# Performance work log

Hardware: AMD Instinct MI355X
Metric: run time of the kernel (lower is better)

Reference implementation:

```python
import jax, jax.numpy as jnp
import numpy as np

D_MODEL = 768; D_KV = 64; H = 12; D_FF = 3072; L = 2
TP = 4; SP = 16; MT = 16; MS = 4
MASK_RATE = 0.2; EPS = 1e-6
B = 256; T = 64; F = 64
ST = (T // TP) * (F // SP)  # 64 tokens


def ln(x, s, b):
    mu = jnp.mean(x, -1, keepdims=True)
    var = jnp.mean(jnp.square(x - mu), -1, keepdims=True)
    return (x - mu) * jax.lax.rsqrt(var + EPS) * s + b


def mha(x, Wq, bq, Wk, bk, Wv, bv, Wo, bo):
    Bz, S, D = x.shape
    q = (x @ Wq + bq).reshape(Bz, S, H, D_KV)
    k = (x @ Wk + bk).reshape(Bz, S, H, D_KV)
    v = (x @ Wv + bv).reshape(Bz, S, H, D_KV)
    scores = jnp.einsum('bqhd,bkhd->bhqk', q, k) * (D_KV ** -0.5)
    attn = jax.nn.softmax(scores, axis=-1)
    o = jnp.einsum('bhqk,bkhd->bqhd', attn, v).reshape(Bz, S, H * D_KV)
    return o @ Wo + bo


def setup_inputs():
    key = jax.random.key(0)
    ks = jax.random.split(key, 16)
    s = 0.02
    nrm = lambda k, shp: jax.random.normal(k, shp, jnp.float32) * s
    return {
        'inputs': jax.random.normal(ks[0], (B, T, F, 1), jnp.float32),
        'randomness': jax.random.uniform(ks[1], (B * ST, 3), jnp.float32),
        'perm': jax.random.permutation(ks[2], B * ST),
        'conv_w': nrm(ks[3], (TP, SP, 1, D_MODEL)), 'conv_b': jnp.zeros((D_MODEL,)),
        'temp_embd': nrm(ks[4], (MT, D_MODEL)), 'spec_embd': nrm(ks[5], (MS, D_MODEL)),
        'pos_ln_s': jnp.ones((D_MODEL,)), 'pos_ln_b': jnp.zeros((D_MODEL,)),
        'mask_tok': nrm(ks[6], (D_MODEL,)), 'agg_tok': nrm(ks[7], (D_MODEL,)),
        'Wq': nrm(ks[8], (L, D_MODEL, H * D_KV)), 'bq': jnp.zeros((L, H * D_KV)),
        'Wk': nrm(ks[9], (L, D_MODEL, H * D_KV)), 'bk': jnp.zeros((L, H * D_KV)),
        'Wv': nrm(ks[10], (L, D_MODEL, H * D_KV)), 'bv': jnp.zeros((L, H * D_KV)),
        'Wo': nrm(ks[11], (L, H * D_KV, D_MODEL)), 'bo': jnp.zeros((L, D_MODEL)),
        'ln1_s': jnp.ones((L, D_MODEL)), 'ln1_b': jnp.zeros((L, D_MODEL)),
        'W1': nrm(ks[12], (L, D_MODEL, D_FF)), 'b1': jnp.zeros((L, D_FF)),
        'W2': nrm(ks[13], (L, D_FF, D_MODEL)), 'b2': jnp.zeros((L, D_MODEL)),
        'ln2_s': jnp.ones((L, D_MODEL)), 'ln2_b': jnp.zeros((L, D_MODEL)),
    }


def reference(inputs, randomness, perm, conv_w, conv_b, temp_embd, spec_embd,
              pos_ln_s, pos_ln_b, mask_tok, agg_tok, Wq, bq, Wk, bk, Wv, bv,
              Wo, bo, ln1_s, ln1_b, W1, b1, W2, b2, ln2_s, ln2_b):
    # Conv2D patchify: [B, T, F, 1] -> [B, T/4, F/16, d_model]
    x = jax.lax.conv_general_dilated(
        inputs, conv_w, (TP, SP), 'VALID',
        dimension_numbers=('NHWC', 'HWIO', 'NHWC')) + conv_b
    Bz, Tt, Ss, D = x.shape
    e = x.reshape(Bz, Tt * Ss, D)  # token embeddings [B, 64, 768]
    # Vectorized BERT-style random masking (replaces the per-element sparse-scatter loop)
    sel = randomness[:, 0] <= MASK_RATE
    m = (sel & (randomness[:, 1] <= 0.8)).astype(e.dtype).reshape(Bz, Tt * Ss)
    rnd = (sel & (randomness[:, 1] > 0.8) & (randomness[:, 2] <= 0.5)).astype(e.dtype).reshape(Bz, Tt * Ss)
    shuffled = jax.lax.stop_gradient(e.reshape(-1, D))[perm].reshape(Bz, Tt * Ss, D)
    me = e * (1.0 - m - rnd)[..., None] + mask_tok * m[..., None] + shuffled * rnd[..., None]
    # Spectro-temporal position embeddings + LN
    pos = (temp_embd[:Tt, None, :] + spec_embd[None, :Ss, :]).reshape(Tt * Ss, D)
    h = ln(me + pos, pos_ln_s, pos_ln_b)
    # Prepend AGG token
    h = jnp.concatenate([jnp.broadcast_to(agg_tok, (Bz, 1, D)), h], axis=1)
    # Post-norm transformer encoder
    for l in range(L):
        a = mha(h, Wq[l], bq[l], Wk[l], bk[l], Wv[l], bv[l], Wo[l], bo[l])
        h = ln(h + a, ln1_s[l], ln1_b[l])
        f = jax.nn.gelu(h @ W1[l] + b1[l], approximate=False) @ W2[l] + b2[l]
        h = ln(h + f, ln2_s[l], ln2_b[l])
    return h  # last_hidden_states [B, 65, 768]; aggregated=h[:,0], predictions=h[:,1:]
```

## Files before the change

kernel.cpp:

```cpp
#include <hip/hip_runtime.h>
#include <hip/hip_bf16.h>
#include <math.h>

using bf16 = __hip_bfloat16;
typedef __bf16 bf16x8v __attribute__((ext_vector_type(8)));
typedef float f32x4 __attribute__((ext_vector_type(4)));
typedef unsigned short ushort4v __attribute__((ext_vector_type(4)));
typedef unsigned short ushort8v __attribute__((ext_vector_type(8)));

__device__ __forceinline__ float b2f(bf16 x) { return __bfloat162float(x); }
__device__ __forceinline__ bf16 f2b(float x) { return __float2bfloat16(x); }

__device__ __forceinline__ void gload_lds16(const void* g, void* l) {
  __builtin_amdgcn_global_load_lds(
      (__attribute__((address_space(1))) void*)(void*)g,
      (__attribute__((address_space(3))) void*)l, 16, 0, 0);
}

__device__ __forceinline__ float block_sum(float v, float* buf) {
  #pragma unroll
  for (int off = 32; off > 0; off >>= 1) v += __shfl_xor(v, off);
  __syncthreads();
  if ((threadIdx.x & 63) == 0) buf[threadIdx.x >> 6] = v;
  __syncthreads();
  return buf[0] + buf[1] + buf[2] + buf[3];
}

__global__ __launch_bounds__(256) void transpose_all_kernel(
    const float* __restrict__ Wq, const float* __restrict__ Wk,
    const float* __restrict__ Wv, const float* __restrict__ Wo,
    const float* __restrict__ W1, const float* __restrict__ W2,
    bf16* __restrict__ wqkvT, bf16* __restrict__ woT,
    bf16* __restrict__ w1T, bf16* __restrict__ w2T) {
  __shared__ float tile[32][33];
  const int tb = blockIdx.x;
  const float* src; bf16* dst; int K, N, t;
  if (tb < 4608) {
    const int job = tb / 576; t = tb % 576;
    const int l = job >> 2, c = job & 3;
    src = (c == 0 ? Wq : c == 1 ? Wk : c == 2 ? Wv : Wo) + (size_t)l * 768 * 768;
    dst = (c < 3) ? (wqkvT + (size_t)l * 2304 * 768 + (size_t)c * 768 * 768)
                  : (woT + (size_t)l * 768 * 768);
    K = 768; N = 768;
  } else if (tb < 9216) {
    const int r = tb - 4608; const int l = r / 2304; t = r % 2304;
    src = W1 + (size_t)l * 768 * 3072; dst = w1T + (size_t)l * 3072 * 768;
    K = 768; N = 3072;
  } else {
    const int r = tb - 9216; const int l = r / 2304; t = r % 2304;
    src = W2 + (size_t)l * 3072 * 768; dst = w2T + (size_t)l * 768 * 3072;
    K = 3072; N = 768;
  }
  const int nbx = N >> 5;
  const int bx = t % nbx, by = t / nbx;
  const int tx = threadIdx.x & 31, ty = threadIdx.x >> 5;
  #pragma unroll
  for (int i = 0; i < 4; ++i) {
    const int r = by * 32 + ty + i * 8;
    tile[ty + i * 8][tx] = src[(size_t)r * N + bx * 32 + tx];
  }
  __syncthreads();
  #pragma unroll
  for (int i = 0; i < 4; ++i) {
    const int r = bx * 32 + ty + i * 8;
    dst[(size_t)r * K + by * 32 + tx] = f2b(tile[tx][ty + i * 8]);
  }
}

__global__ __launch_bounds__(256) void biasqkv_kernel(
    const float* __restrict__ bq, const float* __restrict__ bk,
    const float* __restrict__ bv, float* __restrict__ out) {
  const int i = blockIdx.x * 256 + threadIdx.x;
  if (i >= 2 * 2304) return;
  const int l = i / 2304, n = i % 2304;
  float v = (n < 768) ? bq[l * 768 + n]
          : (n < 1536) ? bk[l * 768 + n - 768] : bv[l * 768 + n - 1536];
  out[i] = v;
}

__global__ __launch_bounds__(256) void patchify_kernel(
    const float* __restrict__ in, const float* __restrict__ w,
    const float* __restrict__ cb, bf16* __restrict__ e) {
  __shared__ float patch[8][64];
  const int tid = threadIdx.x;
  const int tok0 = blockIdx.x * 8;
  for (int idx = tid; idx < 512; idx += 256) {
    const int t = idx >> 6, p = idx & 63;
    const int tok = tok0 + t;
    const int b = tok >> 6, t2 = tok & 63, tt = t2 >> 2, ss = t2 & 3;
    const int kt = p >> 4, kf = p & 15;
    patch[t][p] = in[((size_t)b * 64 + tt * 4 + kt) * 64 + ss * 16 + kf];
  }
  __syncthreads();
  for (int i = 0; i < 3; ++i) {
    const int d = tid + i * 256;
    const float cbv = cb[d];
    float acc[8];
    #pragma unroll
    for (int t = 0; t < 8; ++t) acc[t] = cbv;
    for (int p = 0; p < 64; ++p) {
      const float wv = w[p * 768 + d];
      #pragma unroll
      for (int t = 0; t < 8; ++t) acc[t] += patch[t][p] * wv;
    }
    #pragma unroll
    for (int t = 0; t < 8; ++t) e[(size_t)(tok0 + t) * 768 + d] = f2b(acc[t]);
  }
}

__global__ __launch_bounds__(256) void embed_kernel(
    const bf16* __restrict__ e, const float* __restrict__ randomness,
    const int* __restrict__ perm, const float* __restrict__ temp_embd,
    const float* __restrict__ spec_embd, const float* __restrict__ pls,
    const float* __restrict__ plb, const float* __restrict__ mask_tok,
    const float* __restrict__ agg_tok, bf16* __restrict__ h) {
  __shared__ float rbuf[4];
  const int row = blockIdx.x;
  const int b = row / 65, s = row % 65;
  const int tid = threadIdx.x;
  const size_t ob = (size_t)row * 768;
  if (s == 0) {
    #pragma unroll
    for (int i = 0; i < 3; ++i) { const int d = tid + i * 256; h[ob + d] = f2b(agg_tok[d]); }
    return;
  }
  const int tok = s - 1;
  const int gt = b * 64 + tok;
  const float r0 = randomness[gt * 3 + 0];
  const float r1 = randomness[gt * 3 + 1];
  const float r2 = randomness[gt * 3 + 2];
  const bool selb = (r0 <= 0.2f);
  const bool mflag = selb && (r1 <= 0.8f);
  const bool rflag = selb && (r1 > 0.8f) && (r2 <= 0.5f);
  const int src = rflag ? perm[gt] : gt;
  const int tt = tok >> 2, ss2 = tok & 3;
  float v[3]; float sum = 0.f;
  #pragma unroll
  for (int i = 0; i < 3; ++i) {
    const int d = tid + i * 256;
    const float ev = mflag ? mask_tok[d] : b2f(e[(size_t)src * 768 + d]);
    v[i] = ev + temp_embd[tt * 768 + d] + spec_embd[ss2 * 768 + d];
    sum += v[i];
  }
  const float mu = block_sum(sum, rbuf) * (1.f / 768.f);
  float q = 0.f;
  #pragma unroll
  for (int i = 0; i < 3; ++i) { const float t = v[i] - mu; q += t * t; }
  const float rstd = rsqrtf(block_sum(q, rbuf) * (1.f / 768.f) + 1e-6f);
  #pragma unroll
  for (int i = 0; i < 3; ++i) {
    const int d = tid + i * 256;
    h[ob + d] = f2b((v[i] - mu) * rstd * pls[d] + plb[d]);
  }
}

template <int F32OUT>
__global__ __launch_bounds__(256) void resln_kernel(
    const bf16* __restrict__ x, const bf16* __restrict__ y,
    const float* __restrict__ sc, const float* __restrict__ bi,
    void* __restrict__ outp) {
  __shared__ float rbuf[4];
  const int tid = threadIdx.x;
  const size_t base = (size_t)blockIdx.x * 768;
  float v[3]; float s = 0.f;
  #pragma unroll
  for (int i = 0; i < 3; ++i) {
    const int d = tid + i * 256;
    v[i] = b2f(x[base + d]) + b2f(y[base + d]);
    s += v[i];
  }
  const float mu = block_sum(s, rbuf) * (1.f / 768.f);
  float q = 0.f;
  #pragma unroll
  for (int i = 0; i < 3; ++i) { const float t = v[i] - mu; q += t * t; }
  const float rstd = rsqrtf(block_sum(q, rbuf) * (1.f / 768.f) + 1e-6f);
  #pragma unroll
  for (int i = 0; i < 3; ++i) {
    const int d = tid + i * 256;
    const float o = (v[i] - mu) * rstd * sc[d] + bi[d];
    if (F32OUT) ((float*)outp)[base + d] = o;
    else        ((bf16*)outp)[base + d] = f2b(o);
  }
}

template <int ACT>
__global__ __launch_bounds__(256, 4) void gemm128_kernel(
    const unsigned short* __restrict__ A, const unsigned short* __restrict__ BT,
    const float* __restrict__ bias, bf16* __restrict__ C, int N, int K, int nbn) {
  constexpr int SLOT = 16384;
  __shared__ __align__(16) char smem[2 * SLOT];

  const int nwg = gridDim.x;
  const int orig = blockIdx.x;
  const int q8 = nwg >> 3, r8 = nwg & 7;
  const int xcd = orig & 7, lin = orig >> 3;
  const int bid = (xcd < r8 ? xcd * (q8 + 1) : r8 * (q8 + 1) + (xcd - r8) * q8) + lin;
  const int bm = bid / nbn, bn = bid % nbn;

  const int tid = threadIdx.x;
  const int w = tid >> 6, lane = tid & 63;
  const int wm = (w >> 1) * 64, wn = (w & 1) * 64;
  const int frow = lane & 15;
  const int cg = lane >> 4;
  const int rdCB = ((cg ^ ((frow >> 1) & 3)) << 4);

  const size_t Kb = (size_t)K * 2;
  const int srow = lane >> 2;
  const int srcCB = (((lane & 3) ^ ((lane >> 3) & 3)) << 4);
  const char* gA = (const char*)A + ((size_t)bm * 128 + w * 16 + srow) * Kb + srcCB;
  const char* gB = (const char*)BT + ((size_t)bn * 128 + w * 16 + srow) * Kb + srcCB;

  f32x4 acc[4][4];
  #pragma unroll
  for (int i = 0; i < 4; ++i)
    #pragma unroll
    for (int j = 0; j < 4; ++j) acc[i][j] = f32x4{0.f, 0.f, 0.f, 0.f};

  auto stage = [&](int t, int slotIdx) {
    char* sa = smem + slotIdx * SLOT;
    char* sb = sa + 8192;
    const size_t kb = (size_t)t * 64;
    gload_lds16(gA + kb, sa + w * 1024);
    gload_lds16(gA + (size_t)64 * Kb + kb, sa + 4096 + w * 1024);
    gload_lds16(gB + kb, sb + w * 1024);
    gload_lds16(gB + (size_t)64 * Kb + kb, sb + 4096 + w * 1024);
  };

  auto compute = [&](int slotIdx) {
    const char* sa = smem + slotIdx * SLOT;
    const char* sb = sa + 8192;
    bf16x8v aa[4], bb[4];
    #pragma unroll
    for (int m = 0; m < 4; ++m)
      aa[m] = *(const bf16x8v*)(sa + (wm + m * 16 + frow) * 64 + rdCB);
    #pragma unroll
    for (int n = 0; n < 4; ++n)
      bb[n] = *(const bf16x8v*)(sb + (wn + n * 16 + frow) * 64 + rdCB);
    __builtin_amdgcn_s_setprio(1);
    #pragma unroll
    for (int m = 0; m < 4; ++m)
      #pragma unroll
      for (int n = 0; n < 4; ++n)
        acc[m][n] = __builtin_amdgcn_mfma_f32_16x16x32_bf16(aa[m], bb[n], acc[m][n], 0, 0, 0);
    __builtin_amdgcn_s_setprio(0);
  };

  const int T = K >> 5;
  stage(0, 0);
  __syncthreads();
  int cur = 0;
  for (int t = 0; t < T; ++t) {
    if (t + 1 < T) stage(t + 1, cur ^ 1);
    compute(cur);
    __syncthreads();
    cur ^= 1;
  }

  bf16* cbuf = (bf16*)smem;
  float bias4[4];
  #pragma unroll
  for (int n = 0; n < 4; ++n) bias4[n] = bias[bn * 128 + wn + n * 16 + frow];
  const int rgrp = (lane >> 4) << 2;
  #pragma unroll
  for (int half = 0; half < 2; ++half) {
    if ((w >> 1) == half) {
      #pragma unroll
      for (int mf = 0; mf < 4; ++mf)
        #pragma unroll
        for (int n = 0; n < 4; ++n) {
          const int col = wn + n * 16 + frow;
          #pragma unroll
          for (int r = 0; r < 4; ++r) {
            float v = acc[mf][n][r] + bias4[n];
            if (ACT == 1) v = 0.5f * v * (1.0f + erff(v * 0.70710678f));
            cbuf[(mf * 16 + rgrp + r) * 136 + col] = f2b(v);
          }
        }
    }
    __syncthreads();
    #pragma unroll
    for (int jj = 0; jj < 4; ++jj) {
      const int idx = tid + jj * 256;
      const int rowl = idx >> 4, c = idx & 15;
      const ushort8v val = *(const ushort8v*)(cbuf + rowl * 136 + c * 8);
      *(ushort8v*)(C + ((size_t)(bm * 128 + half * 64 + rowl)) * N + (size_t)bn * 128 + c * 8) = val;
    }
    __syncthreads();
  }
}

__global__ __launch_bounds__(320) void attn_mfma_kernel(
    const bf16* __restrict__ qkv, bf16* __restrict__ ctx) {
  __shared__ __align__(16) bf16 sK[80][72];
  __shared__ __align__(16) bf16 sVt[64][104];
  __shared__ __align__(16) bf16 sP[5][16][104];
  const int b = blockIdx.x / 12, h = blockIdx.x % 12;
  const int tid = threadIdx.x;
  const int wave = tid >> 6, lane = tid & 63;
  const size_t base = ((size_t)b * 65) * 2304 + (size_t)h * 64;
  const bf16 bzero = f2b(0.f);

  for (int idx = tid; idx < 65 * 16; idx += 320) {
    const int row = idx >> 4, d4 = (idx & 15) * 4;
    const ushort4v kv = *(const ushort4v*)(qkv + base + (size_t)row * 2304 + 768 + d4);
    const ushort4v vv = *(const ushort4v*)(qkv + base + (size_t)row * 2304 + 1536 + d4);
    *(ushort4v*)&sK[row][d4] = kv;
    #pragma unroll
    for (int j = 0; j < 4; ++j) ((unsigned short*)&sVt[d4 + j][row])[0] = vv[j];
  }
  for (int idx = tid; idx < 15 * 16; idx += 320) {
    const int row = 65 + (idx >> 4), d4 = (idx & 15) * 4;
    *(ushort4v*)&sK[row][d4] = ushort4v{0, 0, 0, 0};
  }
  for (int idx = tid; idx < 64 * 31; idx += 320) {
    const int d = idx / 31, c = 65 + (idx % 31);
    sVt[d][c] = bzero;
  }
  __syncthreads();

  const int frow = lane & 15;
  const int koff = (lane >> 4) * 8;
  const int row0 = wave * 16;
  const int qrow = (row0 + frow > 64) ? 64 : (row0 + frow);
  const bf16* qptr = qkv + base + (size_t)qrow * 2304;
  const bf16x8v aq0 = *(const bf16x8v*)(qptr + koff);
  const bf16x8v aq1 = *(const bf16x8v*)(qptr + 32 + koff);

  const f32x4 z4 = {0.f, 0.f, 0.f, 0.f};
  f32x4 sacc[5];
  #pragma unroll
  for (int n = 0; n < 5; ++n) sacc[n] = z4;
  #pragma unroll
  for (int n = 0; n < 5; ++n) {
    const bf16x8v b0 = *(const bf16x8v*)&sK[n * 16 + frow][koff];
    const bf16x8v b1 = *(const bf16x8v*)&sK[n * 16 + frow][32 + koff];
    sacc[n] = __builtin_amdgcn_mfma_f32_16x16x32_bf16(aq0, b0, sacc[n], 0, 0, 0);
    sacc[n] = __builtin_amdgcn_mfma_f32_16x16x32_bf16(aq1, b1, sacc[n], 0, 0, 0);
  }

  #pragma unroll
  for (int r = 0; r < 4; ++r) {
    const int prow = ((lane >> 4) << 2) + r;
    float v[5];
    float mx = -1e30f;
    #pragma unroll
    for (int n = 0; n < 5; ++n) {
      const int col = n * 16 + frow;
      v[n] = (col < 65) ? sacc[n][r] * 0.125f : -1e30f;
      mx = fmaxf(mx, v[n]);
    }
    #pragma unroll
    for (int off = 1; off < 16; off <<= 1) mx = fmaxf(mx, __shfl_xor(mx, off));
    float sum = 0.f;
    #pragma unroll
    for (int n = 0; n < 5; ++n) { v[n] = __expf(v[n] - mx); sum += v[n]; }
    #pragma unroll
    for (int off = 1; off < 16; off <<= 1) sum += __shfl_xor(sum, off);
    const float inv = 1.f / sum;
    #pragma unroll
    for (int n = 0; n < 5; ++n)
      sP[wave][prow][n * 16 + frow] = f2b(v[n] * inv);
    sP[wave][prow][80 + frow] = bzero;
  }

  f32x4 oacc[4];
  #pragma unroll
  for (int n = 0; n < 4; ++n) oacc[n] = z4;
  #pragma unroll
  for (int kk = 0; kk < 3; ++kk) {
    const bf16x8v ap = *(const bf16x8v*)&sP[wave][frow][kk * 32 + koff];
    #pragma unroll
    for (int n = 0; n < 4; ++n) {
      const bf16x8v bv = *(const bf16x8v*)&sVt[n * 16 + frow][kk * 32 + koff];
      oacc[n] = __builtin_amdgcn_mfma_f32_16x16x32_bf16(ap, bv, oacc[n], 0, 0, 0);
    }
  }

  #pragma unroll
  for (int r = 0; r < 4; ++r) {
    const int row = row0 + ((lane >> 4) << 2) + r;
    if (row < 65) {
      bf16* op = ctx + ((size_t)b * 65 + row) * 768 + (size_t)h * 64 + frow;
      #pragma unroll
      for (int n = 0; n < 4; ++n) op[n * 16] = f2b(oacc[n][r]);
    }
  }
}

extern "C" void kernel_launch(void* const* d_in, const int* in_sizes, int n_in,
                              void* d_out, int out_size, void* d_ws, size_t ws_size,
                              hipStream_t stream) {
  (void)in_sizes; (void)n_in; (void)out_size; (void)ws_size;
  const float* inputs     = (const float*)d_in[0];
  const float* randomness = (const float*)d_in[1];
  const int*   perm       = (const int*)d_in[2];
  const float* conv_w     = (const float*)d_in[3];
  const float* conv_b     = (const float*)d_in[4];
  const float* temp_embd  = (const float*)d_in[5];
  const float* spec_embd  = (const float*)d_in[6];
  const float* pos_ln_s   = (const float*)d_in[7];
  const float* pos_ln_b   = (const float*)d_in[8];
  const float* mask_tok   = (const float*)d_in[9];
  const float* agg_tok    = (const float*)d_in[10];
  const float* Wq = (const float*)d_in[11]; const float* bq = (const float*)d_in[12];
  const float* Wk = (const float*)d_in[13]; const float* bk = (const float*)d_in[14];
  const float* Wv = (const float*)d_in[15]; const float* bv = (const float*)d_in[16];
  const float* Wo = (const float*)d_in[17]; const float* bo = (const float*)d_in[18];
  const float* ln1_s = (const float*)d_in[19]; const float* ln1_b = (const float*)d_in[20];
  const float* W1 = (const float*)d_in[21]; const float* b1 = (const float*)d_in[22];
  const float* W2 = (const float*)d_in[23]; const float* b2 = (const float*)d_in[24];
  const float* ln2_s = (const float*)d_in[25]; const float* ln2_b = (const float*)d_in[26];

  char* wsb = (char*)d_ws;
  size_t off = 0;
  auto carve = [&](size_t bytes) { char* p = wsb + off; off = (off + bytes + 255) & ~(size_t)255; return p; };
  bf16* wqkvT = (bf16*)carve((size_t)2 * 2304 * 768 * 2);
  bf16* woT   = (bf16*)carve((size_t)2 * 768 * 768 * 2);
  bf16* w1T   = (bf16*)carve((size_t)2 * 3072 * 768 * 2);
  bf16* w2T   = (bf16*)carve((size_t)2 * 768 * 3072 * 2);
  float* bqkv = (float*)carve((size_t)2 * 2304 * 4);
  bf16* ebuf  = (bf16*)carve((size_t)16640 * 768 * 2);
  bf16* hbuf  = (bf16*)carve((size_t)16640 * 768 * 2);
  bf16* qkvb  = (bf16*)carve((size_t)16640 * 2304 * 2);
  bf16* ctxb  = (bf16*)carve((size_t)16640 * 768 * 2);
  bf16* tmpb  = ebuf;
  bf16* midb  = qkvb;

  const dim3 blk(256);
  transpose_all_kernel<<<13824, blk, 0, stream>>>(Wq, Wk, Wv, Wo, W1, W2,
                                                  wqkvT, woT, w1T, w2T);
  biasqkv_kernel<<<18, blk, 0, stream>>>(bq, bk, bv, bqkv);
  patchify_kernel<<<2048, blk, 0, stream>>>(inputs, conv_w, conv_b, ebuf);
  embed_kernel<<<16640, blk, 0, stream>>>(ebuf, randomness, perm, temp_embd, spec_embd,
                                          pos_ln_s, pos_ln_b, mask_tok, agg_tok, hbuf);
  for (int l = 0; l < 2; ++l) {
    gemm128_kernel<0><<<130 * 18, blk, 0, stream>>>(
        (const unsigned short*)hbuf, (const unsigned short*)(wqkvT + (size_t)l * 2304 * 768),
        bqkv + l * 2304, qkvb, 2304, 768, 18);
    attn_mfma_kernel<<<256 * 12, dim3(320), 0, stream>>>(qkvb, ctxb);
    gemm128_kernel<0><<<130 * 6, blk, 0, stream>>>(
        (const unsigned short*)ctxb, (const unsigned short*)(woT + (size_t)l * 768 * 768),
        bo + l * 768, tmpb, 768, 768, 6);
    resln_kernel<0><<<16640, blk, 0, stream>>>(hbuf, tmpb, ln1_s + l * 768, ln1_b + l * 768, hbuf);
    gemm128_kernel<1><<<130 * 24, blk, 0, stream>>>(
        (const unsigned short*)hbuf, (const unsigned short*)(w1T + (size_t)l * 3072 * 768),
        b1 + l * 3072, midb, 3072, 768, 24);
    gemm128_kernel<0><<<130 * 6, blk, 0, stream>>>(
        (const unsigned short*)midb, (const unsigned short*)(w2T + (size_t)l * 768 * 3072),
        b2 + l * 768, tmpb, 768, 3072, 6);
    if (l == 1)
      resln_kernel<1><<<16640, blk, 0, stream>>>(hbuf, tmpb, ln2_s + l * 768, ln2_b + l * 768, d_out);
    else
      resln_kernel<0><<<16640, blk, 0, stream>>>(hbuf, tmpb, ln2_s + l * 768, ln2_b + l * 768, hbuf);
  }
}
```

Measured before the change: 949.9 us.

## Add 256x256-tile 8-wave pipelined GEMM for QKV and FFN1 projections

Introduces a 512-thread GEMM kernel with 256x256 output tiles, a 128KB double-buffered LDS staging scheme, and interleaved async global-to-LDS loads spread across MFMA phases with explicit waitcnt and barriers. It replaces the 128x128 GEMM for the wide QKV and FFN-up projections. The aim is higher arithmetic intensity and better overlap of loads with MFMA work. The cost is lower occupancy and fewer workgroups (585 and 780), which may leave the tail underused on a device with many CUs. The epilogue goes through LDS in two halves.

```diff
diff --git a/kernel.cpp b/kernel.cpp
--- a/kernel.cpp
+++ b/kernel.cpp
@@ -184,6 +184,141 @@
 }
 
 template <int ACT>
+__global__ __launch_bounds__(512, 2) void gemm8p2_kernel(
+    const unsigned short* __restrict__ A, const unsigned short* __restrict__ BT,
+    const float* __restrict__ bias, bf16* __restrict__ C, int N, int K, int nbn) {
+  __shared__ __align__(16) char smem[131072];
+
+  const int nwg = gridDim.x;
+  const int orig = blockIdx.x;
+  const int q8 = nwg >> 3, r8 = nwg & 7;
+  const int xcd = orig & 7, lin = orig >> 3;
+  const int bid = (xcd < r8 ? xcd * (q8 + 1) : r8 * (q8 + 1) + (xcd - r8) * q8) + lin;
+  const int bm = bid / nbn, bn = bid % nbn;
+
+  const int tid = threadIdx.x;
+  const int w = tid >> 6, lane = tid & 63;
+  const int wrow = w >> 2, wcol = w & 3;
+  const int frow = lane & 15;
+  const int cg = lane >> 4;
+  const int rdCB = ((cg ^ ((frow >> 1) & 3)) << 4);
+
+  const size_t Kb = (size_t)K * 2;
+  const int g_lr = lane >> 2;
+  const int srcCB = (((lane & 3) ^ ((lane >> 3) & 3)) << 4);
+  const char* gA = (const char*)A + ((size_t)bm * 256 + w * 16 + g_lr) * Kb + srcCB;
+  const char* gB = (const char*)BT + ((size_t)bn * 256 + w * 16 + g_lr) * Kb + srcCB;
+
+  f32x4 acc[8][4];
+  #pragma unroll
+  for (int i = 0; i < 8; ++i)
+    #pragma unroll
+    for (int j = 0; j < 4; ++j) acc[i][j] = f32x4{0.f, 0.f, 0.f, 0.f};
+
+  auto stageU = [&](int tc, int isB, int h) {
+    char* dst = smem + (tc & 1) * 65536 + isB * 32768 + h * 16384 + w * 1024;
+    const char* g = (isB ? gB : gA) + (size_t)tc * 128 + (size_t)h * 64;
+    gload_lds16(g, dst);
+    gload_lds16(g + (size_t)128 * Kb, dst + 8192);
+  };
+
+  stageU(0, 0, 0); stageU(0, 0, 1); stageU(0, 1, 0); stageU(0, 1, 1);
+  stageU(1, 1, 0); stageU(1, 1, 1);
+
+  const int nIter = K >> 7;
+  bf16x8v bb[4][2];
+
+  for (int i = 0; i < nIter; ++i) {
+    const int t0 = 2 * i;
+    const bool pf = (i + 1 < nIter);
+    #pragma unroll
+    for (int p = 0; p < 8; ++p) {
+      const int sl = p >> 2;
+      const int q = p & 3;
+      const char* slotp = smem + sl * 65536;
+      bf16x8v aa[2][2];
+      if (q == 0) {
+        if (p == 4 && !pf) { asm volatile("s_waitcnt vmcnt(0)" ::: "memory"); }
+        else               { asm volatile("s_waitcnt vmcnt(4)" ::: "memory"); }
+        __builtin_amdgcn_s_barrier();
+        #pragma unroll
+        for (int n = 0; n < 4; ++n) {
+          const int row = wcol * 64 + n * 16 + frow;
+          bb[n][0] = *(const bf16x8v*)(slotp + 32768 + row * 64 + rdCB);
+          bb[n][1] = *(const bf16x8v*)(slotp + 49152 + row * 64 + rdCB);
+        }
+        #pragma unroll
+        for (int j = 0; j < 2; ++j) {
+          const int row = wrow * 128 + j * 16 + frow;
+          aa[j][0] = *(const bf16x8v*)(slotp + row * 64 + rdCB);
+          aa[j][1] = *(const bf16x8v*)(slotp + 16384 + row * 64 + rdCB);
+        }
+        if (p == 0) stageU(t0 + 1, 0, 0);
+        else if (pf) stageU(t0 + 2, 0, 0);
+      } else {
+        #pragma unroll
+        for (int j = 0; j < 2; ++j) {
+          const int row = wrow * 128 + q * 32 + j * 16 + frow;
+          aa[j][0] = *(const bf16x8v*)(slotp + row * 64 + rdCB);
+          aa[j][1] = *(const bf16x8v*)(slotp + 16384 + row * 64 + rdCB);
+        }
+        if (p == 1) stageU(t0 + 1, 0, 1);
+        else if (p == 2) { if (pf) stageU(t0 + 2, 1, 0); }
+        else if (p == 3) { if (pf) stageU(t0 + 2, 1, 1); }
+        else if (p == 5) { if (pf) stageU(t0 + 2, 0, 1); }
+        else if (p == 6) { if (pf) stageU(t0 + 3, 1, 0); }
+        else             { if (pf) stageU(t0 + 3, 1, 1); }
+        __builtin_amdgcn_s_barrier();
+      }
+      asm volatile("s_waitcnt lgkmcnt(0)" ::: "memory");
+      __builtin_amdgcn_sched_barrier(0);
+      __builtin_amdgcn_s_setprio(1);
+      #pragma unroll
+      for (int j = 0; j < 2; ++j)
+        #pragma unroll
+        for (int n = 0; n < 4; ++n) {
+          acc[q * 2 + j][n] = __builtin_amdgcn_mfma_f32_16x16x32_bf16(aa[j][0], bb[n][0], acc[q * 2 + j][n], 0, 0, 0);
+          acc[q * 2 + j][n] = __builtin_amdgcn_mfma_f32_16x16x32_bf16(aa[j][1], bb[n][1], acc[q * 2 + j][n], 0, 0, 0);
+        }
+      __builtin_amdgcn_s_setprio(0);
+    }
+  }
+  __syncthreads();
+
+  bf16* cbuf = (bf16*)smem;
+  float bias4[4];
+  #pragma unroll
+  for (int n = 0; n < 4; ++n) bias4[n] = bias[bn * 256 + wcol * 64 + n * 16 + frow];
+  const int rgrp = (lane >> 4) << 2;
+  #pragma unroll
+  for (int half = 0; half < 2; ++half) {
+    if (wrow == half) {
+      #pragma unroll
+      for (int mf = 0; mf < 8; ++mf)
+        #pragma unroll
+        for (int n = 0; n < 4; ++n) {
+          const int col = wcol * 64 + n * 16 + frow;
+          #pragma unroll
+          for (int r = 0; r < 4; ++r) {
+            float v = acc[mf][n][r] + bias4[n];
+            if (ACT == 1) v = 0.5f * v * (1.0f + erff(v * 0.70710678f));
+            cbuf[(mf * 16 + rgrp + r) * 264 + col] = f2b(v);
+          }
+        }
+    }
+    __syncthreads();
+    #pragma unroll
+    for (int jj = 0; jj < 8; ++jj) {
+      const int idx = tid + jj * 512;
+      const int rowl = idx >> 5, c = idx & 31;
+      const ushort8v val = *(const ushort8v*)(cbuf + rowl * 264 + c * 8);
+      *(ushort8v*)(C + ((size_t)(bm * 256 + half * 128 + rowl)) * N + (size_t)bn * 256 + c * 8) = val;
+    }
+    __syncthreads();
+  }
+}
+
+template <int ACT>
 __global__ __launch_bounds__(256, 4) void gemm128_kernel(
     const unsigned short* __restrict__ A, const unsigned short* __restrict__ BT,
     const float* __restrict__ bias, bf16* __restrict__ C, int N, int K, int nbn) {
@@ -434,17 +569,17 @@
   embed_kernel<<<16640, blk, 0, stream>>>(ebuf, randomness, perm, temp_embd, spec_embd,
                                           pos_ln_s, pos_ln_b, mask_tok, agg_tok, hbuf);
   for (int l = 0; l < 2; ++l) {
-    gemm128_kernel<0><<<130 * 18, blk, 0, stream>>>(
+    gemm8p2_kernel<0><<<65 * 9, dim3(512), 0, stream>>>(
         (const unsigned short*)hbuf, (const unsigned short*)(wqkvT + (size_t)l * 2304 * 768),
-        bqkv + l * 2304, qkvb, 2304, 768, 18);
+        bqkv + l * 2304, qkvb, 2304, 768, 9);
     attn_mfma_kernel<<<256 * 12, dim3(320), 0, stream>>>(qkvb, ctxb);
     gemm128_kernel<0><<<130 * 6, blk, 0, stream>>>(
         (const unsigned short*)ctxb, (const unsigned short*)(woT + (size_t)l * 768 * 768),
         bo + l * 768, tmpb, 768, 768, 6);
     resln_kernel<0><<<16640, blk, 0, stream>>>(hbuf, tmpb, ln1_s + l * 768, ln1_b + l * 768, hbuf);
-    gemm128_kernel<1><<<130 * 24, blk, 0, stream>>>(
+    gemm8p2_kernel<1><<<65 * 12, dim3(512), 0, stream>>>(
         (const unsigned short*)hbuf, (const unsigned short*)(w1T + (size_t)l * 3072 * 768),
-        b1 + l * 3072, midb, 3072, 768, 24);
+        b1 + l * 3072, midb, 3072, 768, 12);
     gemm128_kernel<0><<<130 * 6, blk, 0, stream>>>(
         (const unsigned short*)midb, (const unsigned short*)(w2T + (size_t)l * 768 * 3072),
         b2 + l * 768, tmpb, 768, 3072, 6);
```

Result: slower. 1.096 ms (+15.4%).

## Add 256x128-tile GEMM using 32x32x16 MFMA for QKV and FFN1 projections

Applied to the files above, without the earlier changes.

Adds a new GEMM kernel with a 256x128 output tile per workgroup. Each wave computes a 128x64 sub-tile using 32x32x16 bf16 MFMA instructions, with K-step 32 double-buffered through LDS via direct global-to-LDS loads. It replaces the 128x128 GEMM for the QKV and W1 (GELU) projections, aiming for more operand reuse per LDS byte and fewer, larger MFMA ops. The cost is more accumulator registers and lower occupancy (launch bounds 2), plus a two-pass epilogue that stages output through shared memory.

```diff
diff --git a/kernel.cpp b/kernel.cpp
--- a/kernel.cpp
+++ b/kernel.cpp
@@ -5,6 +5,7 @@
 using bf16 = __hip_bfloat16;
 typedef __bf16 bf16x8v __attribute__((ext_vector_type(8)));
 typedef float f32x4 __attribute__((ext_vector_type(4)));
+typedef float f32x16 __attribute__((ext_vector_type(16)));
 typedef unsigned short ushort4v __attribute__((ext_vector_type(4)));
 typedef unsigned short ushort8v __attribute__((ext_vector_type(8)));
 
@@ -184,6 +185,128 @@
 }
 
 template <int ACT>
+__global__ __launch_bounds__(256, 2) void gemm32_kernel(
+    const unsigned short* __restrict__ A, const unsigned short* __restrict__ BT,
+    const float* __restrict__ bias, bf16* __restrict__ C, int N, int K, int nbn) {
+  constexpr int ABYTES = 256 * 64;
+  constexpr int BBYTES = 128 * 64;
+  constexpr int SLOT = ABYTES + BBYTES;
+  __shared__ __align__(16) char smem[2 * SLOT];
+
+  const int nwg = gridDim.x;
+  const int orig = blockIdx.x;
+  const int q8 = nwg >> 3, r8 = nwg & 7;
+  const int xcd = orig & 7, lin = orig >> 3;
+  const int bid = (xcd < r8 ? xcd * (q8 + 1) : r8 * (q8 + 1) + (xcd - r8) * q8) + lin;
+  const int bm = bid / nbn, bn = bid % nbn;
+
+  const int tid = threadIdx.x;
+  const int w = tid >> 6, lane = tid & 63;
+  const int wrow = w >> 1, wcol = w & 1;
+  const int lrow = lane & 31;
+  const int khl = lane >> 5;
+
+  const size_t Kb = (size_t)K * 2;
+  const int g_lr = lane >> 2;
+  const int srcCB = (((lane & 3) ^ ((lane >> 3) & 3)) << 4);
+  const char* gA = (const char*)A + ((size_t)bm * 256 + w * 16 + g_lr) * Kb + srcCB;
+  const char* gB = (const char*)BT + ((size_t)bn * 128 + w * 16 + g_lr) * Kb + srcCB;
+
+  f32x16 acc[4][2];
+  #pragma unroll
+  for (int i = 0; i < 4; ++i)
+    #pragma unroll
+    for (int j = 0; j < 2; ++j)
+      #pragma unroll
+      for (int r = 0; r < 16; ++r) acc[i][j][r] = 0.f;
+
+  auto stage = [&](int t, int slotIdx) {
+    char* sa = smem + slotIdx * SLOT;
+    char* sb = sa + ABYTES;
+    const size_t kb = (size_t)t * 64;
+    #pragma unroll
+    for (int j = 0; j < 4; ++j)
+      gload_lds16(gA + (size_t)j * 64 * Kb + kb, sa + j * 4096 + w * 1024);
+    #pragma unroll
+    for (int j = 0; j < 2; ++j)
+      gload_lds16(gB + (size_t)j * 64 * Kb + kb, sb + j * 4096 + w * 1024);
+  };
+
+  auto compute = [&](int slotIdx) {
+    const char* sa = smem + slotIdx * SLOT;
+    const char* sb = sa + ABYTES;
+    __builtin_amdgcn_s_setprio(1);
+    #pragma unroll
+    for (int h = 0; h < 2; ++h) {
+      bf16x8v aa[4], bb[2];
+      #pragma unroll
+      for (int mi = 0; mi < 4; ++mi) {
+        const int row = wrow * 128 + mi * 32 + lrow;
+        const int chunk = (h * 2 + khl) ^ ((row >> 1) & 3);
+        aa[mi] = *(const bf16x8v*)(sa + row * 64 + chunk * 16);
+      }
+      #pragma unroll
+      for (int ni = 0; ni < 2; ++ni) {
+        const int row = wcol * 64 + ni * 32 + lrow;
+        const int chunk = (h * 2 + khl) ^ ((row >> 1) & 3);
+        bb[ni] = *(const bf16x8v*)(sb + row * 64 + chunk * 16);
+      }
+      #pragma unroll
+      for (int mi = 0; mi < 4; ++mi)
+        #pragma unroll
+        for (int ni = 0; ni < 2; ++ni)
+          acc[mi][ni] = __builtin_amdgcn_mfma_f32_32x32x16_bf16(
+              aa[mi], bb[ni], acc[mi][ni], 0, 0, 0);
+    }
+    __builtin_amdgcn_s_setprio(0);
+  };
+
+  const int T = K >> 5;
+  stage(0, 0);
+  __syncthreads();
+  int cur = 0;
+  for (int t = 0; t < T; ++t) {
+    if (t + 1 < T) stage(t + 1, cur ^ 1);
+    compute(cur);
+    __syncthreads();
+    cur ^= 1;
+  }
+
+  bf16* cbuf = (bf16*)smem;
+  float bias2[2];
+  #pragma unroll
+  for (int ni = 0; ni < 2; ++ni)
+    bias2[ni] = bias[bn * 128 + wcol * 64 + ni * 32 + lrow];
+  #pragma unroll
+  for (int half = 0; half < 2; ++half) {
+    if (wrow == half) {
+      #pragma unroll
+      for (int mi = 0; mi < 4; ++mi)
+        #pragma unroll
+        for (int ni = 0; ni < 2; ++ni) {
+          const int col = wcol * 64 + ni * 32 + lrow;
+          #pragma unroll
+          for (int r = 0; r < 16; ++r) {
+            const int rowf = (r & 3) + 8 * (r >> 2) + 4 * khl;
+            float v = acc[mi][ni][r] + bias2[ni];
+            if (ACT == 1) v = 0.5f * v * (1.0f + erff(v * 0.70710678f));
+            cbuf[(mi * 32 + rowf) * 136 + col] = f2b(v);
+          }
+        }
+    }
+    __syncthreads();
+    #pragma unroll
+    for (int jj = 0; jj < 8; ++jj) {
+      const int idx = tid + jj * 256;
+      const int rowl = idx >> 4, c = idx & 15;
+      const ushort8v val = *(const ushort8v*)(cbuf + rowl * 136 + c * 8);
+      *(ushort8v*)(C + ((size_t)(bm * 256 + half * 128 + rowl)) * N + (size_t)bn * 128 + c * 8) = val;
+    }
+    __syncthreads();
+  }
+}
+
+template <int ACT>
 __global__ __launch_bounds__(256, 4) void gemm128_kernel(
     const unsigned short* __restrict__ A, const unsigned short* __restrict__ BT,
     const float* __restrict__ bias, bf16* __restrict__ C, int N, int K, int nbn) {
@@ -434,7 +557,7 @@
   embed_kernel<<<16640, blk, 0, stream>>>(ebuf, randomness, perm, temp_embd, spec_embd,
                                           pos_ln_s, pos_ln_b, mask_tok, agg_tok, hbuf);
   for (int l = 0; l < 2; ++l) {
-    gemm128_kernel<0><<<130 * 18, blk, 0, stream>>>(
+    gemm32_kernel<0><<<65 * 18, blk, 0, stream>>>(
         (const unsigned short*)hbuf, (const unsigned short*)(wqkvT + (size_t)l * 2304 * 768),
         bqkv + l * 2304, qkvb, 2304, 768, 18);
     attn_mfma_kernel<<<256 * 12, dim3(320), 0, stream>>>(qkvb, ctxb);
@@ -442,7 +565,7 @@
         (const unsigned short*)ctxb, (const unsigned short*)(woT + (size_t)l * 768 * 768),
         bo + l * 768, tmpb, 768, 768, 6);
     resln_kernel<0><<<16640, blk, 0, stream>>>(hbuf, tmpb, ln1_s + l * 768, ln1_b + l * 768, hbuf);
-    gemm128_kernel<1><<<130 * 24, blk, 0, stream>>>(
+    gemm32_kernel<1><<<65 * 24, blk, 0, stream>>>(
         (const unsigned short*)hbuf, (const unsigned short*)(w1T + (size_t)l * 3072 * 768),
         b1 + l * 3072, midb, 3072, 768, 24);
     gemm128_kernel<0><<<130 * 6, blk, 0, stream>>>(
```

Result: slower. 1.139 ms (+19.9%).

## Switch GEMM to single-buffered BK=64 tiles with 8-way XOR swizzle

Applied to the files above, without the earlier changes.

The GEMM kernel's K-tile grows from 32 to 64, and the double-buffered pipeline is replaced by one 32KB buffer holding A and B tiles. Each iteration now loads, syncs, computes two MFMA k-steps, then syncs again, and the LDS layout uses a 128-byte row with an 8-way XOR swizzle. This halves the number of loop iterations and barriers per unit of K. In exchange, global loads no longer overlap compute within a block, so the kernel relies on the four blocks per CU to hide that latency.

```diff
diff --git a/kernel.cpp b/kernel.cpp
--- a/kernel.cpp
+++ b/kernel.cpp
@@ -184,11 +184,10 @@
 }
 
 template <int ACT>
-__global__ __launch_bounds__(256, 4) void gemm128_kernel(
+__global__ __launch_bounds__(256, 4) void gemmbk64_kernel(
     const unsigned short* __restrict__ A, const unsigned short* __restrict__ BT,
     const float* __restrict__ bias, bf16* __restrict__ C, int N, int K, int nbn) {
-  constexpr int SLOT = 16384;
-  __shared__ __align__(16) char smem[2 * SLOT];
+  __shared__ __align__(16) char smem[32768];
 
   const int nwg = gridDim.x;
   const int orig = blockIdx.x;
@@ -202,13 +201,12 @@
   const int wm = (w >> 1) * 64, wn = (w & 1) * 64;
   const int frow = lane & 15;
   const int cg = lane >> 4;
-  const int rdCB = ((cg ^ ((frow >> 1) & 3)) << 4);
 
   const size_t Kb = (size_t)K * 2;
-  const int srow = lane >> 2;
-  const int srcCB = (((lane & 3) ^ ((lane >> 3) & 3)) << 4);
-  const char* gA = (const char*)A + ((size_t)bm * 128 + w * 16 + srow) * Kb + srcCB;
-  const char* gB = (const char*)BT + ((size_t)bn * 128 + w * 16 + srow) * Kb + srcCB;
+  const int laneRow8 = lane >> 3;
+  const int srcCB = (((lane & 7) ^ laneRow8) << 4);
+  const char* gA = (const char*)A + ((size_t)bm * 128 + w * 32 + laneRow8) * Kb + srcCB;
+  const char* gB = (const char*)BT + ((size_t)bn * 128 + w * 32 + laneRow8) * Kb + srcCB;
 
   f32x4 acc[4][4];
   #pragma unroll
@@ -216,44 +214,48 @@
     #pragma unroll
     for (int j = 0; j < 4; ++j) acc[i][j] = f32x4{0.f, 0.f, 0.f, 0.f};
 
-  auto stage = [&](int t, int slotIdx) {
-    char* sa = smem + slotIdx * SLOT;
-    char* sb = sa + 8192;
-    const size_t kb = (size_t)t * 64;
-    gload_lds16(gA + kb, sa + w * 1024);
-    gload_lds16(gA + (size_t)64 * Kb + kb, sa + 4096 + w * 1024);
-    gload_lds16(gB + kb, sb + w * 1024);
-    gload_lds16(gB + (size_t)64 * Kb + kb, sb + 4096 + w * 1024);
+  char* sa = smem;
+  char* sb = smem + 16384;
+
+  auto stage = [&](int t) {
+    const size_t kb = (size_t)t * 128;
+    #pragma unroll
+    for (int j = 0; j < 4; ++j) {
+      gload_lds16(gA + (size_t)j * 8 * Kb + kb, sa + (w * 32 + j * 8) * 128);
+      gload_lds16(gB + (size_t)j * 8 * Kb + kb, sb + (w * 32 + j * 8) * 128);
+    }
   };
 
-  auto compute = [&](int slotIdx) {
-    const char* sa = smem + slotIdx * SLOT;
-    const char* sb = sa + 8192;
-    bf16x8v aa[4], bb[4];
-    #pragma unroll
-    for (int m = 0; m < 4; ++m)
-      aa[m] = *(const bf16x8v*)(sa + (wm + m * 16 + frow) * 64 + rdCB);
-    #pragma unroll
-    for (int n = 0; n < 4; ++n)
-      bb[n] = *(const bf16x8v*)(sb + (wn + n * 16 + frow) * 64 + rdCB);
-    __builtin_amdgcn_s_setprio(1);
-    #pragma unroll
-    for (int m = 0; m < 4; ++m)
-      #pragma unroll
-      for (int n = 0; n < 4; ++n)
-        acc[m][n] = __builtin_amdgcn_mfma_f32_16x16x32_bf16(aa[m], bb[n], acc[m][n], 0, 0, 0);
-    __builtin_amdgcn_s_setprio(0);
+  auto compute = [&]() {
+    #pragma unroll
+    for (int kk = 0; kk < 2; ++kk) {
+      bf16x8v aa[4], bb[4];
+      #pragma unroll
+      for (int m = 0; m < 4; ++m) {
+        const int row = wm + m * 16 + frow;
+        aa[m] = *(const bf16x8v*)(sa + row * 128 + (((4 * kk + cg) ^ (row & 7)) << 4));
+      }
+      #pragma unroll
+      for (int n = 0; n < 4; ++n) {
+        const int row = wn + n * 16 + frow;
+        bb[n] = *(const bf16x8v*)(sb + row * 128 + (((4 * kk + cg) ^ (row & 7)) << 4));
+      }
+      __builtin_amdgcn_s_setprio(1);
+      #pragma unroll
+      for (int m = 0; m < 4; ++m)
+        #pragma unroll
+        for (int n = 0; n < 4; ++n)
+          acc[m][n] = __builtin_amdgcn_mfma_f32_16x16x32_bf16(aa[m], bb[n], acc[m][n], 0, 0, 0);
+      __builtin_amdgcn_s_setprio(0);
+    }
   };
 
-  const int T = K >> 5;
-  stage(0, 0);
-  __syncthreads();
-  int cur = 0;
+  const int T = K >> 6;
   for (int t = 0; t < T; ++t) {
-    if (t + 1 < T) stage(t + 1, cur ^ 1);
-    compute(cur);
+    stage(t);
     __syncthreads();
-    cur ^= 1;
+    compute();
+    __syncthreads();
   }
 
   bf16* cbuf = (bf16*)smem;
@@ -434,18 +436,18 @@
   embed_kernel<<<16640, blk, 0, stream>>>(ebuf, randomness, perm, temp_embd, spec_embd,
                                           pos_ln_s, pos_ln_b, mask_tok, agg_tok, hbuf);
   for (int l = 0; l < 2; ++l) {
-    gemm128_kernel<0><<<130 * 18, blk, 0, stream>>>(
+    gemmbk64_kernel<0><<<130 * 18, blk, 0, stream>>>(
         (const unsigned short*)hbuf, (const unsigned short*)(wqkvT + (size_t)l * 2304 * 768),
         bqkv + l * 2304, qkvb, 2304, 768, 18);
     attn_mfma_kernel<<<256 * 12, dim3(320), 0, stream>>>(qkvb, ctxb);
-    gemm128_kernel<0><<<130 * 6, blk, 0, stream>>>(
+    gemmbk64_kernel<0><<<130 * 6, blk, 0, stream>>>(
         (const unsigned short*)ctxb, (const unsigned short*)(woT + (size_t)l * 768 * 768),
         bo + l * 768, tmpb, 768, 768, 6);
     resln_kernel<0><<<16640, blk, 0, stream>>>(hbuf, tmpb, ln1_s + l * 768, ln1_b + l * 768, hbuf);
-    gemm128_kernel<1><<<130 * 24, blk, 0, stream>>>(
+    gemmbk64_kernel<1><<<130 * 24, blk, 0, stream>>>(
         (const unsigned short*)hbuf, (const unsigned short*)(w1T + (size_t)l * 3072 * 768),
         b1 + l * 3072, midb, 3072, 768, 24);
-    gemm128_kernel<0><<<130 * 6, blk, 0, stream>>>(
+    gemmbk64_kernel<0><<<130 * 6, blk, 0, stream>>>(
         (const unsigned short*)midb, (const unsigned short*)(w2T + (size_t)l * 768 * 3072),
         b2 + l * 768, tmpb, 768, 3072, 6);
     if (l == 1)
```

Measured after the change: 870.6 us. -8.4%, faster.
